# Kernel tuning notes

Hardware: AMD Instinct MI355X
Metric: run time of the kernel (lower is better)

Reference implementation:

```python
import jax, jax.numpy as jnp
import numpy as np


def setup_inputs() -> dict:
    key = jax.random.key(0)
    ks = jax.random.split(key, 8)
    B, T, F, H, O = 512, 128, 512, 512, 256
    s = 0.05
    return {
        "states": jax.random.normal(ks[0], (B, T, F), jnp.float32),
        "terminated": jax.random.bernoulli(ks[1], 0.02, (B, T)),
        "h0": jnp.zeros((B, H), jnp.float32),
        "W_ih": jax.random.normal(ks[2], (H, F), jnp.float32) * s,
        "W_hh": jax.random.normal(ks[3], (H, H), jnp.float32) * s,
        "b_ih": jax.random.normal(ks[4], (H,), jnp.float32) * s,
        "b_hh": jax.random.normal(ks[5], (H,), jnp.float32) * s,
        "fc_w": jax.random.normal(ks[6], (O, H), jnp.float32) * s,
        "fc_b": jax.random.normal(ks[7], (O,), jnp.float32) * s,
    }


def reference(states, terminated, h0, W_ih, W_hh, b_ih, b_hh, fc_w, fc_b):
    # states: [B, T, F]; terminated: [B, T] bool; h0: [B, H] (num_layers=1)
    B, T, F = states.shape
    # Precompute the input projection once (big GEMM outside the scan).
    x_proj = jnp.einsum("btf,hf->bth", states, W_ih) + b_ih + b_hh  # [B, T, H]
    x_proj_t = jnp.swapaxes(x_proj, 0, 1)          # [T, B, H]
    term_t = jnp.swapaxes(terminated, 0, 1)        # [T, B]

    def step(h, inp):
        xp, tm = inp                               # xp: [B, H], tm: [B]
        h_new = jnp.tanh(xp + h @ W_hh.T)          # vanilla RNN (tanh) cell
        # Zero hidden state of envs that terminated at this step (applied
        # AFTER emitting the output, matching the torch segment-reset logic).
        h_next = jnp.where(tm[:, None], jnp.zeros_like(h_new), h_new)
        return h_next, h_new

    h_final, outs = jax.lax.scan(step, h0, (x_proj_t, term_t))  # outs: [T, B, H]
    rnn_output = jnp.swapaxes(outs, 0, 1).reshape(B * T, -1)    # [B*T, H]
    logits = rnn_output @ fc_w.T + fc_b                          # [B*T, O]
    return logits, h_final
```

## Files before the change

### kernel.cpp

```cpp
#include <hip/hip_runtime.h>
#include <hip/hip_bf16.h>
#include <hip/hip_fp16.h>


typedef _Float16 half8 __attribute__((ext_vector_type(8)));
typedef _Float16 half4 __attribute__((ext_vector_type(4)));
typedef float f32x4 __attribute__((ext_vector_type(4)));

#define XPW_OFF   0UL
#define WIH_OFF   67108864UL
#define FCW_OFF   67633152UL
#define BIAS_OFF  67895296UL
#define WRESA_OFF 67897344UL
#define WRESL_OFF 68290560UL


#define LDS_BARRIER()                                              \
    do {                                                           \
        __builtin_amdgcn_sched_barrier(0);                         \
        asm volatile("s_waitcnt lgkmcnt(0)" ::: "memory");         \
        __builtin_amdgcn_s_barrier();                              \
        __builtin_amdgcn_sched_barrier(0);                         \
    } while (0)

__global__ void conv_w(const float* __restrict__ Wih, const float* __restrict__ Whh,
                       const float* __restrict__ fcw, const float* __restrict__ bih,
                       const float* __restrict__ bhh,
                       _Float16* __restrict__ wih_h, _Float16* __restrict__ fcw_h,
                       float* __restrict__ bias2,
                       _Float16* __restrict__ wresA, _Float16* __restrict__ wresL) {
    int idx = blockIdx.x * 256 + threadIdx.x;
    if (idx < 262144) wih_h[idx] = (_Float16)Wih[idx];
    if (idx < 196608) {
        const int i = idx & 7, l = (idx >> 3) & 63, s = (idx >> 9) & 15;
        const int rest = idx >> 13;
        const int w = rest / 3, nt = rest % 3;
        const int row = w * 64 + (l & 15) * 4 + nt;
        wresA[idx] = (_Float16)Whh[(size_t)row * 512 + s * 32 + (l >> 4) * 8 + i];
    }
    if (idx < 65536) {
        const int i = idx & 7, l = (idx >> 3) & 63, s = (idx >> 9) & 15, w = idx >> 13;
        const int row = w * 64 + (l & 15) * 4 + 3;
        wresL[idx] = (_Float16)Whh[(size_t)row * 512 + s * 32 + (l >> 4) * 8 + i];
    }
    if (idx < 131072) fcw_h[idx] = (_Float16)fcw[idx];
    if (idx < 512) bias2[idx] = bih[idx] + bhh[idx];
}

__global__ __launch_bounds__(256) void gemm_xproj(const float* __restrict__ A,
                                                  const _Float16* __restrict__ Bw,
                                                  const float* __restrict__ bias2,
                                                  _Float16* __restrict__ out) {
    __shared__ _Float16 As[128 * 32];
    __shared__ _Float16 Bs[64 * 32];
    __shared__ _Float16 ep[128 * 64];
    const int tid = threadIdx.x;
    const int s_ = blockIdx.x;
    const int z = s_ & 7, k_ = s_ >> 3;
    const int gid = z * 512 + k_;
    const int b = gid >> 3;
    const int wsp = gid & 7;
    const int lane = tid & 63, w1 = tid >> 6;
    const int ln = lane & 15, kg = lane >> 4;

    f32x4 acc[2][4];
#pragma unroll
    for (int m = 0; m < 2; m++)
#pragma unroll
        for (int n = 0; n < 4; n++) acc[m][n] = (f32x4)0.0f;

    const int sr = tid >> 1, sc = (tid & 1) * 16;
    const int sr2 = tid >> 2, sc2 = (tid & 3) * 8;
    const int brow = wsp * 64 + sr2;

    for (int k0 = 0; k0 < 512; k0 += 32) {
        {
            const float* ga = A + (size_t)(b * 128 + sr) * 512 + k0 + sc;
            float4 f0 = *(const float4*)(ga + 0);
            float4 f1 = *(const float4*)(ga + 4);
            float4 f2 = *(const float4*)(ga + 8);
            float4 f3 = *(const float4*)(ga + 12);
            half8 h0, h1;
            h0[0] = (_Float16)f0.x; h0[1] = (_Float16)f0.y; h0[2] = (_Float16)f0.z; h0[3] = (_Float16)f0.w;
            h0[4] = (_Float16)f1.x; h0[5] = (_Float16)f1.y; h0[6] = (_Float16)f1.z; h0[7] = (_Float16)f1.w;
            h1[0] = (_Float16)f2.x; h1[1] = (_Float16)f2.y; h1[2] = (_Float16)f2.z; h1[3] = (_Float16)f2.w;
            h1[4] = (_Float16)f3.x; h1[5] = (_Float16)f3.y; h1[6] = (_Float16)f3.z; h1[7] = (_Float16)f3.w;
            *(half8*)&As[sr * 32 + sc] = h0;
            *(half8*)&As[sr * 32 + sc + 8] = h1;
        }
        *(half8*)&Bs[sr2 * 32 + sc2] = *(const half8*)(Bw + (size_t)brow * 512 + k0 + sc2);
        __syncthreads();
        half8 af[2], bf[4];
#pragma unroll
        for (int m = 0; m < 2; m++) af[m] = *(const half8*)&As[(w1 * 32 + m * 16 + ln) * 32 + kg * 8];
#pragma unroll
        for (int n = 0; n < 4; n++) bf[n] = *(const half8*)&Bs[(n * 16 + ln) * 32 + kg * 8];
#pragma unroll
        for (int m = 0; m < 2; m++)
#pragma unroll
            for (int n = 0; n < 4; n++)
                acc[m][n] = __builtin_amdgcn_mfma_f32_16x16x32_f16(af[m], bf[n], acc[m][n], 0, 0, 0);
        __syncthreads();
    }
    float bv[4];
#pragma unroll
    for (int n = 0; n < 4; n++) bv[n] = bias2[wsp * 64 + n * 16 + ln];
#pragma unroll
    for (int m = 0; m < 2; m++)
#pragma unroll
        for (int q = 0; q < 4; q++) {
            const int t = w1 * 32 + m * 16 + kg * 4 + q;
#pragma unroll
            for (int n = 0; n < 4; n++)
                ep[t * 64 + n * 16 + ln] = (_Float16)(acc[m][n][q] + bv[n]);
        }
    __syncthreads();
    const int bg = b >> 4, kgs = (b >> 2) & 3, qs = b & 3;
    const size_t obase = (size_t)(bg * 128) * 8192 + (size_t)(wsp * 64 + kgs * 16) * 16 + qs * 4;
#pragma unroll
    for (int j = 0; j < 8; j++) {
        const int wid = tid * 8 + j;
        const int t2 = wid >> 4, sln = wid & 15;
        const half4 v = *(const half4*)&ep[t2 * 64 + sln * 4];
        *(half4*)&out[obase + (size_t)t2 * 8192 + sln * 16] = v;
    }
}

__global__ __launch_bounds__(512, 2) void rnn_scan15(
    const _Float16* __restrict__ xps,
    const _Float16* __restrict__ wresA,
    const _Float16* __restrict__ wresL,
    const int* __restrict__ term,
    const float* __restrict__ h0,
    float* dout) {
    __shared__ __align__(16) _Float16 hb[8192];
    __shared__ __align__(16) _Float16 wl[65536];
    __shared__ unsigned int term_lds[16][4];
    const int tid = threadIdx.x;
    const int bg = blockIdx.x;
    const int R0 = bg * 16;
    const int lane = tid & 63, w = tid >> 6;
    const int ln = lane & 15, kg = lane >> 4;
    _Float16* rnn = (_Float16*)dout;

    half8 wf[48];
    {
        const _Float16* wp = wresA + (size_t)w * 24576 + lane * 8;
#pragma unroll
        for (int f = 0; f < 48; f++) wf[f] = *(const half8*)(wp + (size_t)f * 512);
    }
#pragma unroll
    for (int f = 0; f < 48; f++) asm volatile("" : "+a"(wf[f]));

    for (int u = 0; u < 16; u++) {
        const int o = (u * 512 + tid) * 8;
        *(half8*)&wl[o] = *(const half8*)(wresL + o);
    }
    {
        const int r = tid >> 5, c0 = (tid & 31) * 16;
        const float* gh = h0 + (size_t)(R0 + r) * 512 + c0;
        half8 v0, v1;
#pragma unroll
        for (int i = 0; i < 8; i++) { v0[i] = (_Float16)gh[i]; v1[i] = (_Float16)gh[8 + i]; }
        const int kb = c0 >> 3;
        *(half8*)&hb[kb * 128 + r * 8] = v0;
        *(half8*)&hb[(kb + 1) * 128 + r * 8] = v1;
    }
    if (tid < 64) {
        const int r = tid >> 2, word = tid & 3;
        unsigned int m = 0;
        for (int b2 = 0; b2 < 32; b2++)
            m |= (term[(R0 + r) * 128 + word * 32 + b2] ? 1u : 0u) << b2;
        term_lds[r][word] = m;
    }
    __syncthreads();

    const _Float16* xpt = xps + (size_t)(bg * 128) * 8192 + tid * 16;
    const _Float16* bl = &wl[(size_t)w * 8192];
    const int cb = w * 64 + ln * 4;
    const int hoff = (cb >> 3) * 128 + (cb & 7);
    unsigned int tmask[4];

#pragma unroll 1
    for (int t = 0; t < 128; ++t) {
        if ((t & 31) == 0) {
#pragma unroll
            for (int q = 0; q < 4; q++) tmask[q] = term_lds[kg * 4 + q][t >> 5];
        }
        const half8 xv0 = *(const half8*)(xpt);
        const half8 xv1 = *(const half8*)(xpt + 8);
        xpt += 8192;

        f32x4 acc[4];
#pragma unroll
        for (int n = 0; n < 4; n++) acc[n] = (f32x4)0.0f;

#pragma unroll
        for (int s = 0; s < 16; s++) {
            const half8 a = *(const half8*)&hb[(s * 4 + kg) * 128 + ln * 8];
            acc[0] = __builtin_amdgcn_mfma_f32_16x16x32_f16(a, wf[s],      acc[0], 0, 0, 0);
            acc[1] = __builtin_amdgcn_mfma_f32_16x16x32_f16(a, wf[16 + s], acc[1], 0, 0, 0);
            acc[2] = __builtin_amdgcn_mfma_f32_16x16x32_f16(a, wf[32 + s], acc[2], 0, 0, 0);
            const half8 b4 = *(const half8*)(bl + s * 512 + lane * 8);
            acc[3] = __builtin_amdgcn_mfma_f32_16x16x32_f16(a, b4, acc[3], 0, 0, 0);
        }
        LDS_BARRIER();

        half4 hh4[4];
#pragma unroll
        for (int q = 0; q < 4; q++) {
            const bool dead = (tmask[q] >> (t & 31)) & 1;
            half4 v;
#pragma unroll
            for (int nt = 0; nt < 4; nt++) {
                const int u = q * 4 + nt;
                const float xval = (float)(u < 8 ? xv0[u] : xv1[u - 8]);
                const float pre = acc[nt][q] + xval;
                const float e = __expf(2.0f * pre);
                v[nt] = (_Float16)(1.0f - 2.0f * __builtin_amdgcn_rcpf(e + 1.0f));
            }
            hh4[q] = v;
            half4 mv = v;
            if (dead) { mv[0] = (_Float16)0; mv[1] = (_Float16)0; mv[2] = (_Float16)0; mv[3] = (_Float16)0; }
            *(half4*)&hb[hoff + (kg * 4 + q) * 8] = mv;
        }
        LDS_BARRIER();

#pragma unroll
        for (int q = 0; q < 4; q++)
            *(half4*)&rnn[((size_t)(R0 + kg * 4 + q) * 128 + t) * 512 + cb] = hh4[q];
    }

    {
        const int r = tid >> 5, c0 = (tid & 31) * 16;
        const int kb = c0 >> 3;
        half8 v0 = *(const half8*)&hb[kb * 128 + r * 8];
        half8 v1 = *(const half8*)&hb[(kb + 1) * 128 + r * 8];
        float* gf = dout + (size_t)65536 * 256 + (size_t)(R0 + r) * 512 + c0;
#pragma unroll
        for (int i = 0; i < 8; i++) { gf[i] = (float)v0[i]; gf[8 + i] = (float)v1[i]; }
    }
}

__global__ __launch_bounds__(512) void gemm_logits(const _Float16* Arnn,
                                                   const _Float16* __restrict__ Bw,
                                                   const float* __restrict__ biasv,
                                                   float* out) {
    __shared__ _Float16 As[128 * 32];
    __shared__ _Float16 Bs[256 * 32];
    const int tid = threadIdx.x;
    const int m0 = blockIdx.x * 128;
    const int lane = tid & 63, w = tid >> 6;
    const int wr = (w >> 2) * 64, wc = (w & 3) * 64;
    const int ln = lane & 15, kg = lane >> 4;

    f32x4 acc[4][4];
#pragma unroll
    for (int m = 0; m < 4; m++)
#pragma unroll
        for (int n = 0; n < 4; n++) acc[m][n] = (f32x4)0.0f;

    const int ar = tid >> 2, ac = (tid & 3) * 8;
    const int br = tid >> 1, bc = (tid & 1) * 16;

    for (int k0 = 0; k0 < 512; k0 += 32) {
        *(half8*)&As[ar * 32 + ac] = *(const half8*)(Arnn + (size_t)(m0 + ar) * 512 + k0 + ac);
        {
            const _Float16* gb = Bw + (size_t)br * 512 + k0 + bc;
            *(half8*)&Bs[br * 32 + bc] = *(const half8*)(gb);
            *(half8*)&Bs[br * 32 + bc + 8] = *(const half8*)(gb + 8);
        }
        __syncthreads();
        half8 af[4], bf[4];
#pragma unroll
        for (int m = 0; m < 4; m++) af[m] = *(const half8*)&As[(wr + m * 16 + ln) * 32 + kg * 8];
#pragma unroll
        for (int n = 0; n < 4; n++) bf[n] = *(const half8*)&Bs[(wc + n * 16 + ln) * 32 + kg * 8];
#pragma unroll
        for (int m = 0; m < 4; m++)
#pragma unroll
            for (int n = 0; n < 4; n++)
                acc[m][n] = __builtin_amdgcn_mfma_f32_16x16x32_f16(af[m], bf[n], acc[m][n], 0, 0, 0);
        __syncthreads();
    }
#pragma unroll
    for (int m = 0; m < 4; m++)
#pragma unroll
        for (int n = 0; n < 4; n++) {
            const int col = wc + n * 16 + ln;
            const float bv = biasv[col];
#pragma unroll
            for (int q = 0; q < 4; q++) {
                const int row = m0 + wr + m * 16 + kg * 4 + q;
                out[(size_t)row * 256 + col] = acc[m][n][q] + bv;
            }
        }
}

extern "C" void kernel_launch(void* const* d_in, const int* in_sizes, int n_in,
                              void* d_out, int out_size, void* d_ws, size_t ws_size,
                              hipStream_t stream) {
    const float* states = (const float*)d_in[0];
    const int*   term   = (const int*)d_in[1];
    const float* h0     = (const float*)d_in[2];
    const float* Wih    = (const float*)d_in[3];
    const float* Whh    = (const float*)d_in[4];
    const float* bih    = (const float*)d_in[5];
    const float* bhh    = (const float*)d_in[6];
    const float* fcw    = (const float*)d_in[7];
    const float* fcb    = (const float*)d_in[8];

    char* ws = (char*)d_ws;
    _Float16* xpw   = (_Float16*)(ws + XPW_OFF);
    _Float16* wih_h = (_Float16*)(ws + WIH_OFF);
    _Float16* fcw_h = (_Float16*)(ws + FCW_OFF);
    float*    bias2 = (float*)(ws + BIAS_OFF);
    _Float16* wresA = (_Float16*)(ws + WRESA_OFF);
    _Float16* wresL = (_Float16*)(ws + WRESL_OFF);

    conv_w<<<1024, 256, 0, stream>>>(Wih, Whh, fcw, bih, bhh, wih_h, fcw_h, bias2, wresA, wresL);
    gemm_xproj<<<4096, 256, 0, stream>>>(states, wih_h, bias2, xpw);
    rnn_scan15<<<32, 512, 0, stream>>>(xpw, wresA, wresL, term, h0, (float*)d_out);
    gemm_logits<<<512, 512, 0, stream>>>((const _Float16*)d_out, fcw_h, fcb, (float*)d_out);
}
```

Baseline: 429.8 us.

## Widen xproj GEMM tile to 128x128 and pad RNN hidden-state LDS stride

The input-projection GEMM now computes 128x128 output tiles per block instead of 128x64, which halves the grid and re-reads the fp32 states operand half as often. The epilogue scatter is rewritten to match the interleaved layout the scan expects. Separately, the scan kernel's hidden-state LDS buffer row stride is padded from 128 to 136 halves to reduce bank conflicts on the per-step A-fragment reads. The larger tile uses more accumulator registers and more LDS (the epilogue buffer doubles), which may lower occupancy.

```diff
diff --git a/kernel.cpp b/kernel.cpp
--- a/kernel.cpp
+++ b/kernel.cpp
@@ -14,6 +14,8 @@
 #define WRESA_OFF 67897344UL
 #define WRESL_OFF 68290560UL
 
+
+#define HB_STRIDE 136
 
 #define LDS_BARRIER()                                              \
     do {                                                           \
@@ -52,26 +54,26 @@
                                                   const float* __restrict__ bias2,
                                                   _Float16* __restrict__ out) {
     __shared__ _Float16 As[128 * 32];
-    __shared__ _Float16 Bs[64 * 32];
-    __shared__ _Float16 ep[128 * 64];
+    __shared__ _Float16 Bs[128 * 32];
+    __shared__ _Float16 ep[128 * 128];
     const int tid = threadIdx.x;
     const int s_ = blockIdx.x;
     const int z = s_ & 7, k_ = s_ >> 3;
-    const int gid = z * 512 + k_;
-    const int b = gid >> 3;
-    const int wsp = gid & 7;
+    const int gid = z * 256 + k_;
+    const int b = gid >> 2;
+    const int cb2 = gid & 3;
     const int lane = tid & 63, w1 = tid >> 6;
+    const int wr = (w1 >> 1) * 64, wc = (w1 & 1) * 64;
     const int ln = lane & 15, kg = lane >> 4;
 
-    f32x4 acc[2][4];
-#pragma unroll
-    for (int m = 0; m < 2; m++)
+    f32x4 acc[4][4];
+#pragma unroll
+    for (int m = 0; m < 4; m++)
 #pragma unroll
         for (int n = 0; n < 4; n++) acc[m][n] = (f32x4)0.0f;
 
     const int sr = tid >> 1, sc = (tid & 1) * 16;
-    const int sr2 = tid >> 2, sc2 = (tid & 3) * 8;
-    const int brow = wsp * 64 + sr2;
+    const int brow = cb2 * 128 + sr;
 
     for (int k0 = 0; k0 < 512; k0 += 32) {
         {
@@ -88,15 +90,19 @@
             *(half8*)&As[sr * 32 + sc] = h0;
             *(half8*)&As[sr * 32 + sc + 8] = h1;
         }
-        *(half8*)&Bs[sr2 * 32 + sc2] = *(const half8*)(Bw + (size_t)brow * 512 + k0 + sc2);
+        {
+            const _Float16* gb = Bw + (size_t)brow * 512 + k0 + sc;
+            *(half8*)&Bs[sr * 32 + sc] = *(const half8*)(gb);
+            *(half8*)&Bs[sr * 32 + sc + 8] = *(const half8*)(gb + 8);
+        }
         __syncthreads();
-        half8 af[2], bf[4];
-#pragma unroll
-        for (int m = 0; m < 2; m++) af[m] = *(const half8*)&As[(w1 * 32 + m * 16 + ln) * 32 + kg * 8];
-#pragma unroll
-        for (int n = 0; n < 4; n++) bf[n] = *(const half8*)&Bs[(n * 16 + ln) * 32 + kg * 8];
-#pragma unroll
-        for (int m = 0; m < 2; m++)
+        half8 af[4], bf[4];
+#pragma unroll
+        for (int m = 0; m < 4; m++) af[m] = *(const half8*)&As[(wr + m * 16 + ln) * 32 + kg * 8];
+#pragma unroll
+        for (int n = 0; n < 4; n++) bf[n] = *(const half8*)&Bs[(wc + n * 16 + ln) * 32 + kg * 8];
+#pragma unroll
+        for (int m = 0; m < 4; m++)
 #pragma unroll
             for (int n = 0; n < 4; n++)
                 acc[m][n] = __builtin_amdgcn_mfma_f32_16x16x32_f16(af[m], bf[n], acc[m][n], 0, 0, 0);
@@ -104,36 +110,36 @@
     }
     float bv[4];
 #pragma unroll
-    for (int n = 0; n < 4; n++) bv[n] = bias2[wsp * 64 + n * 16 + ln];
-#pragma unroll
-    for (int m = 0; m < 2; m++)
+    for (int n = 0; n < 4; n++) bv[n] = bias2[cb2 * 128 + wc + n * 16 + ln];
+#pragma unroll
+    for (int m = 0; m < 4; m++)
 #pragma unroll
         for (int q = 0; q < 4; q++) {
-            const int t = w1 * 32 + m * 16 + kg * 4 + q;
+            const int t = wr + m * 16 + kg * 4 + q;
 #pragma unroll
             for (int n = 0; n < 4; n++)
-                ep[t * 64 + n * 16 + ln] = (_Float16)(acc[m][n][q] + bv[n]);
+                ep[t * 128 + wc + n * 16 + ln] = (_Float16)(acc[m][n][q] + bv[n]);
         }
     __syncthreads();
     const int bg = b >> 4, kgs = (b >> 2) & 3, qs = b & 3;
-    const size_t obase = (size_t)(bg * 128) * 8192 + (size_t)(wsp * 64 + kgs * 16) * 16 + qs * 4;
-#pragma unroll
-    for (int j = 0; j < 8; j++) {
-        const int wid = tid * 8 + j;
-        const int t2 = wid >> 4, sln = wid & 15;
-        const half4 v = *(const half4*)&ep[t2 * 64 + sln * 4];
-        *(half4*)&out[obase + (size_t)t2 * 8192 + sln * 16] = v;
-    }
-}
-
-__global__ __launch_bounds__(512, 2) void rnn_scan15(
+    const size_t obase = (size_t)(bg * 128) * 8192 + (size_t)(cb2 * 2 * 64 + kgs * 16) * 16 + qs * 4;
+#pragma unroll
+    for (int j = 0; j < 16; j++) {
+        const int wid = j * 256 + tid;
+        const int t2 = wid >> 5, slb = wid & 31;
+        const half4 v = *(const half4*)&ep[t2 * 128 + slb * 4];
+        *(half4*)&out[obase + (size_t)t2 * 8192 + (slb >> 4) * 1024 + (slb & 15) * 16] = v;
+    }
+}
+
+__global__ __launch_bounds__(512, 2) void rnn_scan16(
     const _Float16* __restrict__ xps,
     const _Float16* __restrict__ wresA,
     const _Float16* __restrict__ wresL,
     const int* __restrict__ term,
     const float* __restrict__ h0,
     float* dout) {
-    __shared__ __align__(16) _Float16 hb[8192];
+    __shared__ __align__(16) _Float16 hb[64 * HB_STRIDE];
     __shared__ __align__(16) _Float16 wl[65536];
     __shared__ unsigned int term_lds[16][4];
     const int tid = threadIdx.x;
@@ -163,8 +169,8 @@
 #pragma unroll
         for (int i = 0; i < 8; i++) { v0[i] = (_Float16)gh[i]; v1[i] = (_Float16)gh[8 + i]; }
         const int kb = c0 >> 3;
-        *(half8*)&hb[kb * 128 + r * 8] = v0;
-        *(half8*)&hb[(kb + 1) * 128 + r * 8] = v1;
+        *(half8*)&hb[kb * HB_STRIDE + r * 8] = v0;
+        *(half8*)&hb[(kb + 1) * HB_STRIDE + r * 8] = v1;
     }
     if (tid < 64) {
         const int r = tid >> 2, word = tid & 3;
@@ -178,7 +184,7 @@
     const _Float16* xpt = xps + (size_t)(bg * 128) * 8192 + tid * 16;
     const _Float16* bl = &wl[(size_t)w * 8192];
     const int cb = w * 64 + ln * 4;
-    const int hoff = (cb >> 3) * 128 + (cb & 7);
+    const int hoff = (cb >> 3) * HB_STRIDE + (cb & 7);
     unsigned int tmask[4];
 
 #pragma unroll 1
@@ -197,7 +203,7 @@
 
 #pragma unroll
         for (int s = 0; s < 16; s++) {
-            const half8 a = *(const half8*)&hb[(s * 4 + kg) * 128 + ln * 8];
+            const half8 a = *(const half8*)&hb[(s * 4 + kg) * HB_STRIDE + ln * 8];
             acc[0] = __builtin_amdgcn_mfma_f32_16x16x32_f16(a, wf[s],      acc[0], 0, 0, 0);
             acc[1] = __builtin_amdgcn_mfma_f32_16x16x32_f16(a, wf[16 + s], acc[1], 0, 0, 0);
             acc[2] = __builtin_amdgcn_mfma_f32_16x16x32_f16(a, wf[32 + s], acc[2], 0, 0, 0);
@@ -234,8 +240,8 @@
     {
         const int r = tid >> 5, c0 = (tid & 31) * 16;
         const int kb = c0 >> 3;
-        half8 v0 = *(const half8*)&hb[kb * 128 + r * 8];
-        half8 v1 = *(const half8*)&hb[(kb + 1) * 128 + r * 8];
+        half8 v0 = *(const half8*)&hb[kb * HB_STRIDE + r * 8];
+        half8 v1 = *(const half8*)&hb[(kb + 1) * HB_STRIDE + r * 8];
         float* gf = dout + (size_t)65536 * 256 + (size_t)(R0 + r) * 512 + c0;
 #pragma unroll
         for (int i = 0; i < 8; i++) { gf[i] = (float)v0[i]; gf[8 + i] = (float)v1[i]; }
@@ -319,7 +325,7 @@
     _Float16* wresL = (_Float16*)(ws + WRESL_OFF);
 
     conv_w<<<1024, 256, 0, stream>>>(Wih, Whh, fcw, bih, bhh, wih_h, fcw_h, bias2, wresA, wresL);
-    gemm_xproj<<<4096, 256, 0, stream>>>(states, wih_h, bias2, xpw);
-    rnn_scan15<<<32, 512, 0, stream>>>(xpw, wresA, wresL, term, h0, (float*)d_out);
+    gemm_xproj<<<2048, 256, 0, stream>>>(states, wih_h, bias2, xpw);
+    rnn_scan16<<<32, 512, 0, stream>>>(xpw, wresA, wresL, term, h0, (float*)d_out);
     gemm_logits<<<512, 512, 0, stream>>>((const _Float16*)d_out, fcw_h, fcb, (float*)d_out);
 }
```

Result: faster. 397.3 us (median of 3 runs) (-7.6%).
